# Optimization experiments

Hardware: AMD Instinct MI355X
Metric: run time of the kernel (lower is better)

The kernel has to match this reference:

```python
import jax, jax.numpy as jnp
import numpy as np
import math

B = 8; SEQ = 1000; C_IN = 32; D = 512; H = 8; DK = 64; DV = 64
DFF = 2048; NL = 4; ARY = 4; INNER = 5


def get_mask_np(seq_size, ary, inner):
    # full k-ary tree sizes (padded) and effective sizes per scale
    full = 1
    while full < seq_size:
        full *= ary
    all_size = [full]; effe = [seq_size]
    while all_size[-1] > 1:
        all_size.append(all_size[-1] // ary)
        effe.append(math.ceil(effe[-1] / ary))
    n = sum(all_size)
    allow = np.zeros((n, n), dtype=bool)
    w = inner // 2
    starts = np.concatenate([[0], np.cumsum(all_size)]).astype(int)
    # intra-scale local window
    for l, sz in enumerate(all_size):
        s = starts[l]
        for i in range(sz):
            lo = max(i - w, 0); hi = min(i + w + 1, sz)
            allow[s + i, s + lo:s + hi] = True
    # inter-scale parent<->children links
    for l in range(1, len(all_size)):
        s = starts[l]; ps = starts[l - 1]
        for i in range(all_size[l]):
            lo = ps + i * ary; hi = ps + (i + 1) * ary
            allow[s + i, lo:hi] = True
            allow[lo:hi, s + i] = True
    return allow, all_size, effe

ALLOW_NP, ALL_SIZE, EFFE_SIZE = get_mask_np(SEQ, ARY, INNER)
NTOT = sum(ALL_SIZE)   # 1365
DEPTH = len(ALL_SIZE)  # 6
OFFS = np.concatenate([[0], np.cumsum(ALL_SIZE)]).astype(int)


def sinusoid_pe(length, d):
    pos = np.arange(length)[:, None].astype(np.float64)
    i = np.arange(d)[None, :]
    ang = pos / np.power(10000.0, (2 * (i // 2)) / d)
    pe = np.zeros((length, d), np.float32)
    pe[:, 0::2] = np.sin(ang[:, 0::2]); pe[:, 1::2] = np.cos(ang[:, 1::2])
    return pe

PE_NP = sinusoid_pe(SEQ, D)


def layer_norm(x, s, b, eps=1e-5):
    m = x.mean(-1, keepdims=True)
    v = ((x - m) ** 2).mean(-1, keepdims=True)
    return (x - m) * jax.lax.rsqrt(v + eps) * s + b


def setup_inputs() -> dict:
    key = jax.random.key(0)
    ks = jax.random.split(key, 10)
    p = lambda k, shape, sc=0.02: jax.random.normal(k, shape, jnp.float32) * sc
    return {
        "x": jax.random.normal(ks[0], (B, SEQ, C_IN), jnp.float32),
        "conv_w": p(ks[1], (D, C_IN, 3), 0.05),
        "norm_s": jnp.ones((D,), jnp.float32), "norm_b": jnp.zeros((D,), jnp.float32),
        "wq": p(ks[2], (NL, D, H * DK)), "wk": p(ks[3], (NL, D, H * DK)),
        "wv": p(ks[4], (NL, D, H * DV)), "wo": p(ks[5], (NL, H * DV, D)),
        "ln1_s": jnp.ones((NL, D), jnp.float32), "ln1_b": jnp.zeros((NL, D), jnp.float32),
        "w1": p(ks[6], (NL, D, DFF)), "b1": jnp.zeros((NL, DFF), jnp.float32),
        "w2": p(ks[7], (NL, DFF, D)), "b2": jnp.zeros((NL, D), jnp.float32),
        "ln2_s": jnp.ones((NL, D), jnp.float32), "ln2_b": jnp.zeros((NL, D), jnp.float32),
    }


def reference(x, conv_w, norm_s, norm_b, wq, wk, wv, wo, ln1_s, ln1_b,
              w1, b1, w2, b2, ln2_s, ln2_b):
    allow = jnp.asarray(ALLOW_NP)        # [N,N] True = attend
    pe = jnp.asarray(PE_NP)              # [S,D]
    # --- DataEmbedding: conv1d(k=3, circular pad, no bias) + sinusoid PE ---
    xt = jnp.concatenate([x[:, -1:], x, x[:, :1]], axis=1)       # (B,S+2,C)
    emb = jax.lax.conv_general_dilated(
        xt, conv_w, (1,), 'VALID', dimension_numbers=('NWC', 'OIW', 'NWC'))
    emb = emb + pe[None]                                          # (B,S,D)
    # pad sequence to full-tree leaf count
    emb = jnp.pad(emb, ((0, 0), (0, ALL_SIZE[0] - SEQ), (0, 0)))  # (B,L0,D)
    # --- MaxPooling_Construct: pool by ary per level, concat, LayerNorm ---
    parts = [emb]
    cur = emb
    for lvl in range(DEPTH - 1):
        L = cur.shape[1]
        cur = cur.reshape(B, L // ARY, ARY, D).max(axis=2)
        parts.append(cur)
    seq = jnp.concatenate(parts, axis=1)                          # (B,N,D)
    seq = layer_norm(seq, norm_s, norm_b)
    # --- masked MHA encoder layers (post-norm) ---
    scale = 1.0 / math.sqrt(DK)
    neg = jnp.float32(-1e9)
    for l in range(NL):
        q = (seq @ wq[l]).reshape(B, NTOT, H, DK)
        k = (seq @ wk[l]).reshape(B, NTOT, H, DK)
        v = (seq @ wv[l]).reshape(B, NTOT, H, DV)
        scores = jnp.einsum('bnhd,bmhd->bhnm', q, k) * scale
        scores = jnp.where(allow[None, None], scores, neg)
        attn = jax.nn.softmax(scores, axis=-1)
        ctx = jnp.einsum('bhnm,bmhd->bnhd', attn, v).reshape(B, NTOT, H * DV)
        seq = layer_norm(seq + ctx @ wo[l], ln1_s[l], ln1_b[l])
        ff = jax.nn.gelu(seq @ w1[l] + b1[l], approximate=False) @ w2[l] + b2[l]
        seq = layer_norm(seq + ff, ln2_s[l], ln2_b[l])
    # --- keep only the effective (unpadded) prefix of each scale ---
    out = jnp.concatenate(
        [seq[:, OFFS[i]:OFFS[i] + EFFE_SIZE[i]] for i in range(DEPTH)], axis=1)
    return out  # (B, sum(effe)=1334, D)
```

## Files before the change

kernel.cpp:

```cpp
#include <hip/hip_runtime.h>
#include <cstdint>
#include <math.h>

#define DEV __device__ __forceinline__

static constexpr int BQ = 8, SEQN = 1000, CIN = 32, NH = 8;
static constexpr int NLAY = 4;
static constexpr int NTOT_C = 1365;
static constexpr int M_REAL = BQ * NTOT_C;
static constexpr int M_PAD  = 11008;

DEV float bf2f(unsigned short u){ return __uint_as_float(((unsigned)u) << 16); }
DEV unsigned short f2bf(float f){
  unsigned u = __float_as_uint(f);
  u += 0x7fffu + ((u >> 16) & 1u);
  return (unsigned short)(u >> 16);
}

typedef __bf16 bf16x8 __attribute__((ext_vector_type(8)));
typedef float  f32x4  __attribute__((ext_vector_type(4)));
typedef unsigned short u16x8 __attribute__((ext_vector_type(8)));

#define GLD_LDS16(gp, lp) __builtin_amdgcn_global_load_lds( \
    (const __attribute__((address_space(1))) void*)(gp), \
    (__attribute__((address_space(3))) void*)(lp), 16, 0, 0)

__global__ __launch_bounds__(256) void pe_kernel(float* __restrict__ pe)
{
  int idx = blockIdx.x * 256 + threadIdx.x;
  int d = idx & 511, s = idx >> 9;
  if (s >= SEQN) return;
  float e2 = (float)(d & ~1);
  float freq = exp2f(e2 * (-13.287712379549449f / 512.0f));
  float ang = (float)s * freq;
  pe[idx] = (d & 1) ? cosf(ang) : sinf(ang);
}

__global__ __launch_bounds__(256) void conv_kernel(const float* __restrict__ x,
    const float* __restrict__ w, const float* __restrict__ pe, float* __restrict__ seqf)
{
  __shared__ float ws_w[128 * 97];
  __shared__ __align__(16) float xs[66][32];
  int b = blockIdx.z, s0 = blockIdx.y * 64, d0 = blockIdx.x * 128;
  int tid = threadIdx.x;
  for (int i = tid; i < 128 * 96; i += 256){
    int r = i / 96, c = i - r * 96;
    ws_w[r * 97 + c] = w[(size_t)(d0 + r) * 96 + c];
  }
  for (int i = tid; i < 66 * 32; i += 256){
    int r = i >> 5, c = i & 31;
    int ss = s0 + r - 1;
    ss = (ss < 0) ? (ss + SEQN) : (ss >= SEQN ? ss - SEQN : ss);
    xs[r][c] = x[((size_t)b * SEQN + ss) * CIN + c];
  }
  __syncthreads();
  int dl = tid & 127, sh = tid >> 7;
  float wr[96];
  #pragma unroll
  for (int i = 0; i < 96; i++) wr[i] = ws_w[dl * 97 + i];
  int d = d0 + dl;
  for (int si = 0; si < 32; si++){
    int sl = sh * 32 + si;
    int s = s0 + sl;
    float acc = 0.f;
    #pragma unroll
    for (int kk = 0; kk < 3; kk++){
      const float* xr = xs[sl + kk];
      #pragma unroll
      for (int c = 0; c < 32; c++) acc += xr[c] * wr[c * 3 + kk];
    }
    float outv = (s < SEQN) ? acc + pe[(size_t)s * 512 + d] : 0.f;
    seqf[((size_t)b * NTOT_C + s) * 512 + d] = outv;
  }
}

__global__ __launch_bounds__(256) void pool_kernel(float* __restrict__ seqf,
    int inOff, int outOff, int outSz)
{
  int e = blockIdx.x * 256 + threadIdx.x;
  int d = e & 511;
  int r = e >> 9;
  int i = r % outSz;
  int b = r / outSz;
  const float* src = seqf + ((size_t)b * NTOT_C + inOff + 4 * i) * 512 + d;
  float m = fmaxf(fmaxf(src[0], src[512]), fmaxf(src[1024], src[1536]));
  seqf[((size_t)b * NTOT_C + outOff + i) * 512 + d] = m;
}

template<bool RES>
__global__ __launch_bounds__(256) void ln_kernel(const float* __restrict__ xin,
    const float* __restrict__ rin, float* __restrict__ outf, unsigned short* __restrict__ outb,
    const float* __restrict__ sg, const float* __restrict__ bg, int M)
{
  int row = blockIdx.x;
  int t = threadIdx.x;
  size_t base = (size_t)row * 512;
  if (row >= M){ outb[base + t] = 0; outb[base + t + 256] = 0; return; }
  float v0 = xin[base + t], v1 = xin[base + t + 256];
  if (RES){ v0 += rin[base + t]; v1 += rin[base + t + 256]; }
  __shared__ float red1[4], red2[4];
  int wv = t >> 6;
  float sall = v0 + v1;
  #pragma unroll
  for (int o = 32; o; o >>= 1) sall += __shfl_xor(sall, o, 64);
  if ((t & 63) == 0) red1[wv] = sall;
  __syncthreads();
  float mean = (red1[0] + red1[1] + red1[2] + red1[3]) * (1.f / 512.f);
  float d0 = v0 - mean, d1 = v1 - mean;
  float sq = d0 * d0 + d1 * d1;
  #pragma unroll
  for (int o = 32; o; o >>= 1) sq += __shfl_xor(sq, o, 64);
  if ((t & 63) == 0) red2[wv] = sq;
  __syncthreads();
  float var = (red2[0] + red2[1] + red2[2] + red2[3]) * (1.f / 512.f);
  float rstd = 1.f / sqrtf(var + 1e-5f);
  float y0 = d0 * rstd * sg[t] + bg[t];
  float y1 = d1 * rstd * sg[t + 256] + bg[t + 256];
  outf[base + t] = y0; outf[base + t + 256] = y1;
  outb[base + t] = f2bf(y0); outb[base + t + 256] = f2bf(y1);
}

__global__ __launch_bounds__(256) void wconv_kernel(const float* __restrict__ w,
    unsigned short* __restrict__ wt, int K, int N, size_t sStride, size_t dStride)
{
  __shared__ float tile[32][33];
  const float* wl = w + blockIdx.z * sStride;
  unsigned short* wtl = wt + blockIdx.z * dStride;
  int n0 = blockIdx.x * 32, k0 = blockIdx.y * 32;
  int c = threadIdx.x & 31, r8 = threadIdx.x >> 5;
  #pragma unroll
  for (int p = 0; p < 4; p++){ int r = r8 + p * 8; tile[r][c] = wl[(size_t)(k0 + r) * N + n0 + c]; }
  __syncthreads();
  #pragma unroll
  for (int p = 0; p < 4; p++){ int r = r8 + p * 8; wtl[(size_t)(n0 + r) * K + k0 + c] = f2bf(tile[c][r]); }
}

template<int EPI, int MR, int NR>
__global__ __launch_bounds__(256) void gemm_kernel(
    const unsigned short* __restrict__ A, const unsigned short* __restrict__ Wt,
    float* __restrict__ Cf, unsigned short* __restrict__ Cb,
    const float* __restrict__ bias, const float* __restrict__ Rf, int N, int K)
{
  constexpr int BM = 32 * MR, BN = 32 * NR;
  __shared__ __align__(16) unsigned short As[2][BM * 32];
  __shared__ __align__(16) unsigned short Bs[2][BN * 32];
  const int tid = threadIdx.x;
  const int wv = tid >> 6, lane = tid & 63;
  const int m0 = blockIdx.x * BM, n0 = blockIdx.y * BN;
  const int wm = (wv >> 1) * 16 * MR, wn = (wv & 1) * 16 * NR;
  const int r16 = lane & 15, g = lane >> 4;

  const unsigned short* gA = A + (size_t)(m0 + 8 * MR * wv + (lane >> 2)) * K + (lane & 3) * 8;
  const unsigned short* gB = Wt + (size_t)(n0 + 8 * NR * wv + (lane >> 2)) * K + (lane & 3) * 8;
  const int lAoff = wv * 8 * MR * 32;
  const int lBoff = wv * 8 * NR * 32;

  f32x4 acc[MR][NR] = {};
  const int nt = K >> 5;

  auto STAGE = [&](int buf, int k0){
    #pragma unroll
    for (int ii = 0; ii < MR / 2; ii++)
      GLD_LDS16(gA + k0 + ii * 16 * K, &As[buf][lAoff + ii * 512]);
    #pragma unroll
    for (int ii = 0; ii < NR / 2; ii++)
      GLD_LDS16(gB + k0 + ii * 16 * K, &Bs[buf][lBoff + ii * 512]);
  };

  STAGE(0, 0);
  __syncthreads();
  int cur = 0;
  for (int t = 0; t < nt; t++){
    if (t + 1 < nt) STAGE(cur ^ 1, (t + 1) * 32);
    bf16x8 av[MR], bv[NR];
    #pragma unroll
    for (int m = 0; m < MR; m++)
      av[m] = *reinterpret_cast<const bf16x8*>(&As[cur][(wm + m * 16 + r16) * 32 + g * 8]);
    #pragma unroll
    for (int n = 0; n < NR; n++)
      bv[n] = *reinterpret_cast<const bf16x8*>(&Bs[cur][(wn + n * 16 + r16) * 32 + g * 8]);
    #pragma unroll
    for (int m = 0; m < MR; m++)
      #pragma unroll
      for (int n = 0; n < NR; n++)
        acc[m][n] = __builtin_amdgcn_mfma_f32_16x16x32_bf16(av[m], bv[n], acc[m][n], 0, 0, 0);
    __syncthreads();
    cur ^= 1;
  }

  const int colBase = n0 + wn + r16;
  #pragma unroll
  for (int m = 0; m < MR; m++){
    int rowBase = m0 + wm + m * 16 + g * 4;
    #pragma unroll
    for (int n = 0; n < NR; n++){
      int col = colBase + n * 16;
      float bsv = (EPI >= 2) ? bias[col] : 0.f;
      #pragma unroll
      for (int j = 0; j < 4; j++){
        float vlu = acc[m][n][j];
        if (EPI >= 2) vlu += bsv;
        if (EPI == 2) vlu = 0.5f * vlu * (1.f + erff(vlu * 0.70710678118654752f));
        size_t off = (size_t)(rowBase + j) * N + col;
        if (EPI == 0 || EPI == 3) vlu += Rf[off];
        if (EPI == 1 || EPI == 2) Cb[off] = f2bf(vlu);
        else                      Cf[off] = vlu;
      }
    }
  }
}

__global__ __launch_bounds__(256) void attn_kernel(
    const unsigned short* __restrict__ qkv, unsigned short* __restrict__ ctx)
{
  int wid = blockIdx.x * 4 + (threadIdx.x >> 6);
  int lane = threadIdx.x & 63;
  int n = wid % NTOT_C;
  int b = wid / NTOT_C;

  int i, sz, of, cb, par;
  if (n < 1024){ i = n;        sz = 1024; of = 0;    cb = -1;            par = 1024 + (i >> 2); }
  else if (n < 1280){ i = n - 1024; sz = 256; of = 1024; cb = 0    + 4 * i; par = 1280 + (i >> 2); }
  else if (n < 1344){ i = n - 1280; sz = 64;  of = 1280; cb = 1024 + 4 * i; par = 1344 + (i >> 2); }
  else if (n < 1360){ i = n - 1344; sz = 16;  of = 1344; cb = 1280 + 4 * i; par = 1360 + (i >> 2); }
  else if (n < 1364){ i = n - 1360; sz = 4;   of = 1360; cb = 1344 + 4 * i; par = 1364; }
  else { i = 0; sz = 1; of = 1364; cb = 1360; par = -1; }

  int nb[10];
  #pragma unroll
  for (int s5 = 0; s5 < 5; s5++){ int pos = i - 2 + s5; nb[s5] = (pos >= 0 && pos < sz) ? of + pos : -1; }
  #pragma unroll
  for (int r = 0; r < 4; r++) nb[5 + r] = (cb >= 0) ? cb + r : -1;
  nb[9] = par;

  const unsigned short* rows = qkv + ((size_t)b * NTOT_C) * 1536;

  u16x8 qv = *reinterpret_cast<const u16x8*>(rows + (size_t)n * 1536 + lane * 8);
  float qf[8];
  #pragma unroll
  for (int e = 0; e < 8; e++) qf[e] = bf2f(qv[e]);

  float sc[10];
  #pragma unroll
  for (int j = 0; j < 10; j++){
    int id = nb[j] >= 0 ? nb[j] : n;
    u16x8 kv = *reinterpret_cast<const u16x8*>(rows + (size_t)id * 1536 + 512 + lane * 8);
    float p = 0.f;
    #pragma unroll
    for (int e = 0; e < 8; e++) p += qf[e] * bf2f(kv[e]);
    p += __shfl_xor(p, 1, 64);
    p += __shfl_xor(p, 2, 64);
    p += __shfl_xor(p, 4, 64);
    sc[j] = (nb[j] >= 0) ? p * 0.125f : -1e30f;
  }
  float mx = sc[0];
  #pragma unroll
  for (int j = 1; j < 10; j++) mx = fmaxf(mx, sc[j]);
  float den = 0.f;
  float wj[10];
  #pragma unroll
  for (int j = 0; j < 10; j++){
    wj[j] = (nb[j] >= 0) ? expf(sc[j] - mx) : 0.f;
    den += wj[j];
  }
  float rden = 1.f / den;
  float accv[8] = {};
  #pragma unroll
  for (int j = 0; j < 10; j++){
    int id = nb[j] >= 0 ? nb[j] : n;
    u16x8 vv = *reinterpret_cast<const u16x8*>(rows + (size_t)id * 1536 + 1024 + lane * 8);
    float w = wj[j];
    #pragma unroll
    for (int e = 0; e < 8; e++) accv[e] += w * bf2f(vv[e]);
  }
  u16x8 ov;
  #pragma unroll
  for (int e = 0; e < 8; e++) ov[e] = f2bf(accv[e] * rden);
  *reinterpret_cast<u16x8*>(ctx + ((size_t)b * NTOT_C + n) * 512 + lane * 8) = ov;
}

__global__ __launch_bounds__(256) void gather_kernel(const float* __restrict__ seqf,
    float* __restrict__ out)
{
  int e = blockIdx.x * 256 + threadIdx.x;
  int d = e & 511;
  int r = e >> 9;
  int j = r % 1334;
  int b = r / 1334;
  int src;
  if      (j < 1000) src = j;
  else if (j < 1250) src = j + 24;
  else if (j < 1313) src = j + 30;
  else if (j < 1333) src = j + 31;
  else               src = 1364;
  out[e] = seqf[((size_t)b * NTOT_C + src) * 512 + d];
}

extern "C" void kernel_launch(void* const* d_in, const int* in_sizes, int n_in,
                              void* d_out, int out_size, void* d_ws, size_t ws_size,
                              hipStream_t stream)
{
  const float* x      = (const float*)d_in[0];
  const float* conv_w = (const float*)d_in[1];
  const float* norm_s = (const float*)d_in[2];
  const float* norm_b = (const float*)d_in[3];
  const float* wq     = (const float*)d_in[4];
  const float* wk     = (const float*)d_in[5];
  const float* wv     = (const float*)d_in[6];
  const float* wo     = (const float*)d_in[7];
  const float* ln1_s  = (const float*)d_in[8];
  const float* ln1_b  = (const float*)d_in[9];
  const float* w1     = (const float*)d_in[10];
  const float* b1     = (const float*)d_in[11];
  const float* w2     = (const float*)d_in[12];
  const float* b2     = (const float*)d_in[13];
  const float* ln2_s  = (const float*)d_in[14];
  const float* ln2_b  = (const float*)d_in[15];
  float* out = (float*)d_out;

  char* ws = (char*)d_ws;
  size_t off = 0;
  auto alloc = [&](size_t bytes) -> char* {
    char* p = ws + off; off += (bytes + 255) & ~(size_t)255; return p;
  };
  unsigned short* qkvT = (unsigned short*)alloc((size_t)NLAY * 1536 * 512 * 2);
  unsigned short* woT  = (unsigned short*)alloc((size_t)NLAY * 512 * 512 * 2);
  unsigned short* w1T  = (unsigned short*)alloc((size_t)NLAY * 2048 * 512 * 2);
  unsigned short* w2T  = (unsigned short*)alloc((size_t)NLAY * 512 * 2048 * 2);
  float*          seqf = (float*)alloc((size_t)M_PAD * 512 * 4);
  unsigned short* seqb = (unsigned short*)alloc((size_t)M_PAD * 512 * 2);
  float*          buff = (float*)alloc((size_t)M_PAD * 512 * 4);
  unsigned short* qkvb = (unsigned short*)alloc((size_t)M_PAD * 1536 * 2);
  unsigned short* ctxb = (unsigned short*)alloc((size_t)M_PAD * 512 * 2);
  unsigned short* ffn1 = qkvb;
  float*          pe   = buff;

  wconv_kernel<<<dim3(16,16,NLAY),256,0,stream>>>(wq, qkvT,              512,  512,  (size_t)512*512,  (size_t)1536*512);
  wconv_kernel<<<dim3(16,16,NLAY),256,0,stream>>>(wk, qkvT + 512*512,    512,  512,  (size_t)512*512,  (size_t)1536*512);
  wconv_kernel<<<dim3(16,16,NLAY),256,0,stream>>>(wv, qkvT + 1024*512,   512,  512,  (size_t)512*512,  (size_t)1536*512);
  wconv_kernel<<<dim3(16,16,NLAY),256,0,stream>>>(wo, woT,               512,  512,  (size_t)512*512,  (size_t)512*512);
  wconv_kernel<<<dim3(64,16,NLAY),256,0,stream>>>(w1, w1T,               512,  2048, (size_t)512*2048, (size_t)512*2048);
  wconv_kernel<<<dim3(16,64,NLAY),256,0,stream>>>(w2, w2T,               2048, 512,  (size_t)2048*512, (size_t)2048*512);

  pe_kernel<<<(SEQN * 512) / 256, 256, 0, stream>>>(pe);
  conv_kernel<<<dim3(4,16,BQ), 256, 0, stream>>>(x, conv_w, pe, seqf);
  const int psz[6]  = {1024, 256, 64, 16, 4, 1};
  const int poff[6] = {0, 1024, 1280, 1344, 1360, 1364};
  for (int l = 0; l < 5; l++)
    pool_kernel<<<(BQ * psz[l+1] * 512) / 256, 256, 0, stream>>>(seqf, poff[l], poff[l+1], psz[l+1]);
  ln_kernel<false><<<M_PAD, 256, 0, stream>>>(seqf, nullptr, seqf, seqb, norm_s, norm_b, M_REAL);

  for (int l = 0; l < NLAY; l++){
    gemm_kernel<1,4,4><<<dim3(86,12),256,0,stream>>>(seqb, qkvT + (size_t)l*1536*512, nullptr, qkvb, nullptr, nullptr, 1536, 512);
    attn_kernel<<<(BQ * NTOT_C + 3) / 4, 256, 0, stream>>>(qkvb, ctxb);
    gemm_kernel<0,2,2><<<dim3(172,8),256,0,stream>>>(ctxb, woT + (size_t)l*512*512, buff, nullptr, nullptr, seqf, 512, 512);
    ln_kernel<false><<<M_PAD,256,0,stream>>>(buff, nullptr, seqf, seqb, ln1_s + l*512, ln1_b + l*512, M_REAL);
    gemm_kernel<2,4,4><<<dim3(86,16),256,0,stream>>>(seqb, w1T + (size_t)l*2048*512, nullptr, ffn1, b1 + l*2048, nullptr, 2048, 512);
    gemm_kernel<3,2,4><<<dim3(172,4),256,0,stream>>>(ffn1, w2T + (size_t)l*512*2048, buff, nullptr, b2 + l*512, seqf, 512, 2048);
    ln_kernel<false><<<M_PAD,256,0,stream>>>(buff, nullptr, seqf, seqb, ln2_s + l*512, ln2_b + l*512, M_REAL);
  }

  gather_kernel<<<(BQ * 1334 * 512) / 256, 256, 0, stream>>>(seqf, out);
}
```

Before: 843.7 us.

## Triple-buffer GEMM LDS staging with vmcnt waits, swizzle, and MFMA priority

The GEMM main loop moves from double to triple buffering of the A/B tiles, prefetching two k-steps ahead. It replaces __syncthreads with explicit s_waitcnt vmcnt counts plus s_barrier, so loads for later tiles can stay in flight while the current tile is computed. It also XOR-swizzles the 16-byte column chunks in LDS to reduce bank conflicts on the fragment reads, and raises wave priority around the MFMA block. This costs more shared memory per block, which may lower occupancy, and the hand-counted vmcnt values must match the number of issued loads.

Measured after the change: 838.9 us. About the same (-0.6%).

```diff
diff --git a/kernel.cpp b/kernel.cpp
--- a/kernel.cpp
+++ b/kernel.cpp
@@ -24,6 +24,11 @@
 #define GLD_LDS16(gp, lp) __builtin_amdgcn_global_load_lds( \
     (const __attribute__((address_space(1))) void*)(gp), \
     (__attribute__((address_space(3))) void*)(lp), 16, 0, 0)
+
+template<int N> DEV void waitcnt_vm(){
+  asm volatile("s_waitcnt vmcnt(%0)" :: "i"(N) : "memory");
+}
+DEV void cfence(){ asm volatile("" ::: "memory"); }
 
 __global__ __launch_bounds__(256) void pe_kernel(float* __restrict__ pe)
 {
@@ -142,50 +147,64 @@
     const float* __restrict__ bias, const float* __restrict__ Rf, int N, int K)
 {
   constexpr int BM = 32 * MR, BN = 32 * NR;
-  __shared__ __align__(16) unsigned short As[2][BM * 32];
-  __shared__ __align__(16) unsigned short Bs[2][BN * 32];
+  constexpr int SLOT_A = BM * 32, SLOT_B = BN * 32;
+  constexpr int L = MR / 2 + NR / 2;
+  __shared__ __align__(16) unsigned short As[3][SLOT_A];
+  __shared__ __align__(16) unsigned short Bs[3][SLOT_B];
   const int tid = threadIdx.x;
   const int wv = tid >> 6, lane = tid & 63;
   const int m0 = blockIdx.x * BM, n0 = blockIdx.y * BN;
   const int wm = (wv >> 1) * 16 * MR, wn = (wv & 1) * 16 * NR;
   const int r16 = lane & 15, g = lane >> 4;
 
-  const unsigned short* gA = A + (size_t)(m0 + 8 * MR * wv + (lane >> 2)) * K + (lane & 3) * 8;
-  const unsigned short* gB = Wt + (size_t)(n0 + 8 * NR * wv + (lane >> 2)) * K + (lane & 3) * 8;
+  const int lrow = lane >> 2;
+  const int scg  = (lane & 3) ^ ((lrow >> 1) & 3);
+  const unsigned short* gA = A + (size_t)(m0 + 8 * MR * wv + lrow) * K + scg * 8;
+  const unsigned short* gB = Wt + (size_t)(n0 + 8 * NR * wv + lrow) * K + scg * 8;
   const int lAoff = wv * 8 * MR * 32;
   const int lBoff = wv * 8 * NR * 32;
 
   f32x4 acc[MR][NR] = {};
   const int nt = K >> 5;
 
-  auto STAGE = [&](int buf, int k0){
+  auto STAGE = [&](int slot, int k0){
     #pragma unroll
     for (int ii = 0; ii < MR / 2; ii++)
-      GLD_LDS16(gA + k0 + ii * 16 * K, &As[buf][lAoff + ii * 512]);
+      GLD_LDS16(gA + k0 + ii * 16 * K, &As[slot][lAoff + ii * 512]);
     #pragma unroll
     for (int ii = 0; ii < NR / 2; ii++)
-      GLD_LDS16(gB + k0 + ii * 16 * K, &Bs[buf][lBoff + ii * 512]);
+      GLD_LDS16(gB + k0 + ii * 16 * K, &Bs[slot][lBoff + ii * 512]);
   };
 
   STAGE(0, 0);
-  __syncthreads();
+  STAGE(1, 32);
   int cur = 0;
+  const int rswz = (g ^ ((r16 >> 1) & 3)) * 8;
   for (int t = 0; t < nt; t++){
-    if (t + 1 < nt) STAGE(cur ^ 1, (t + 1) * 32);
+    int s2 = (cur == 0) ? 2 : cur - 1;
+    if (t + 2 < nt) STAGE(s2, (t + 2) * 32);
+    if (t + 2 < nt)      waitcnt_vm<2 * L>();
+    else if (t + 1 < nt) waitcnt_vm<L>();
+    else                 waitcnt_vm<0>();
+    __builtin_amdgcn_s_barrier();
+    cfence();
     bf16x8 av[MR], bv[NR];
     #pragma unroll
     for (int m = 0; m < MR; m++)
-      av[m] = *reinterpret_cast<const bf16x8*>(&As[cur][(wm + m * 16 + r16) * 32 + g * 8]);
+      av[m] = *reinterpret_cast<const bf16x8*>(&As[cur][(wm + m * 16 + r16) * 32 + rswz]);
     #pragma unroll
     for (int n = 0; n < NR; n++)
-      bv[n] = *reinterpret_cast<const bf16x8*>(&Bs[cur][(wn + n * 16 + r16) * 32 + g * 8]);
+      bv[n] = *reinterpret_cast<const bf16x8*>(&Bs[cur][(wn + n * 16 + r16) * 32 + rswz]);
+    __builtin_amdgcn_s_setprio(1);
     #pragma unroll
     for (int m = 0; m < MR; m++)
       #pragma unroll
       for (int n = 0; n < NR; n++)
         acc[m][n] = __builtin_amdgcn_mfma_f32_16x16x32_bf16(av[m], bv[n], acc[m][n], 0, 0, 0);
-    __syncthreads();
-    cur ^= 1;
+    __builtin_amdgcn_s_setprio(0);
+    __builtin_amdgcn_s_barrier();
+    cfence();
+    cur = (cur == 2) ? 0 : cur + 1;
   }
 
   const int colBase = n0 + wn + r16;
```
